# Kernel optimization log

Hardware: AMD Instinct MI355X
Metric: run time of the kernel (lower is better)

## Reference

```python
import jax, jax.numpy as jnp
import numpy as np

N_NODES = 100000
N_TYPES = 7
E_PER_TYPE = 250000
D = 128


def setup_inputs() -> dict:
    key = jax.random.key(0)
    k1, k2, k3 = jax.random.split(key, 3)
    x = jax.random.normal(k1, (N_NODES, D), dtype=jnp.float32)
    edge_index = jax.random.randint(k2, (N_TYPES, 2, E_PER_TYPE), 0, N_NODES, dtype=jnp.int64)
    # per-edge-type GNN weights (SwitchModule holds one param set per type)
    W = jax.random.normal(k3, (N_TYPES, D, D), dtype=jnp.float32) * (1.0 / np.sqrt(D))
    b = jnp.zeros((N_TYPES, D), dtype=jnp.float32)
    return {"x": x, "edge_index": edge_index, "W": W, "b": b}


def reference(x, edge_index, W, b):
    # x: [N, D]; edge_index: [T, 2, E]; W: [T, D, D]; b: [T, D]
    N = x.shape[0]
    E = edge_index.shape[-1]
    # per-type linear transform of all node features: [T, N, D]
    h = jnp.einsum('nd,tdf->tnf', x, W) + b[:, None, :]

    def per_type(ht, ei):
        src, dst = ei[0], ei[1]
        msgs = ht[src]                                   # [E, D] gather
        sums = jax.ops.segment_sum(msgs, dst, num_segments=N)
        cnt = jax.ops.segment_sum(jnp.ones((E,), ht.dtype), dst, num_segments=N)
        return sums / jnp.maximum(cnt, 1.0)[:, None]     # mean aggregation

    type_messages = jax.vmap(per_type)(h, edge_index)    # [T, N, D]
    # x_agg = sum(type_messages) / len(type_messages)
    return type_messages.mean(axis=0)
```

## Files before the change

### kernel.cpp

```cpp
#include <hip/hip_runtime.h>


constexpr int NN = 100000;
constexpr int NT = 7;
constexpr int NE = 250000;
constexpr int DD = 128;
constexpr int NROWS = ((NN + 127) / 128) * 128;
constexpr int NPART = 8;
constexpr int PSIZE = (NN + NPART - 1) / NPART;
constexpr int EPB = 1024;
constexpr int NSLAB = (NE + EPB - 1) / EPB;

typedef short bf16x8 __attribute__((ext_vector_type(8)));
typedef float f32x4 __attribute__((ext_vector_type(4)));
typedef int   i32x4 __attribute__((ext_vector_type(4)));
typedef float fltx4 __attribute__((ext_vector_type(4)));

__device__ __forceinline__ unsigned pack_bf16x2(float lo, float hi) {
    unsigned a = __float_as_uint(lo), b = __float_as_uint(hi);
    unsigned al = (a + 0x7FFFu + ((a >> 16) & 1u)) >> 16;
    unsigned bh = (b + 0x7FFFu + ((b >> 16) & 1u)) & 0xFFFF0000u;
    return al | bh;
}

__global__ __launch_bounds__(256) void convx_k(
    const float* __restrict__ x, uint4* __restrict__ xb)
{
    int id = blockIdx.x * 256 + threadIdx.x;
    const fltx4* src = (const fltx4*)x;
    fltx4 v0 = __builtin_nontemporal_load(src + (size_t)id * 2);
    fltx4 v1 = __builtin_nontemporal_load(src + (size_t)id * 2 + 1);
    uint4 o;
    o.x = pack_bf16x2(v0[0], v0[1]);
    o.y = pack_bf16x2(v0[2], v0[3]);
    o.z = pack_bf16x2(v1[0], v1[1]);
    o.w = pack_bf16x2(v1[2], v1[3]);
    xb[id] = o;
}

__global__ __launch_bounds__(256) void wconv_k(
    const float* __restrict__ W, char* __restrict__ WTb)
{
    int wid = (blockIdx.x * 256 + threadIdx.x) >> 6;
    int lane = threadIdx.x & 63;
    int t = wid >> 7, f = wid & 127;
    if (t >= NT) return;
    const float* Wt = W + (size_t)t * DD * DD;
    float w0 = Wt[(size_t)(2 * lane) * DD + f];
    float w1 = Wt[(size_t)(2 * lane + 1) * DD + f];
    int gran = (lane >> 2) ^ (f & 7);
    *(unsigned*)(WTb + (size_t)t * 32768 + f * 256 + gran * 16 + (lane & 3) * 4)
        = pack_bf16x2(w0, w1);
}

__global__ __launch_bounds__(256) void fill_k(
    const int* __restrict__ ei,
    int* __restrict__ cntT,
    int* __restrict__ eslots)
{
    int part = blockIdx.x & (NPART - 1);
    int slab = blockIdx.x >> 3;
    int t = blockIdx.y;
    int e0 = slab * EPB + threadIdx.x * 4;
    if (e0 >= NE) return;
    const int* p = ei + (size_t)t * 2 * NE;
    i32x4 s4 = __builtin_nontemporal_load((const i32x4*)(p + e0));
    i32x4 d4 = __builtin_nontemporal_load((const i32x4*)(p + NE + e0));
    int lo = part * PSIZE;
    int hi = lo + PSIZE;
    int tv = t << 17;
    #pragma unroll
    for (int k = 0; k < 4; ++k) {
        int src = s4[k];
        int dst = d4[k];
        if (dst >= lo && dst < hi) {
            int pos = atomicAdd(cntT + dst, 1);
            if (pos < 64) eslots[(size_t)dst * 64 + pos] = src | tv;
        }
    }
}

__global__ __launch_bounds__(256) void agg_k(
    const char* __restrict__ xb,
    const int* __restrict__ cntT,
    const int* __restrict__ eslots,
    char* __restrict__ aggb,
    unsigned char* __restrict__ bmask,
    int c0, int nc)
{
    int wid = (blockIdx.x * 256 + threadIdx.x) >> 6;
    int lane = threadIdx.x & 63;
    if (wid >= nc) return;
    const int n = c0 + wid;
    const bool live = (n < NN);

    int total = live ? cntT[n] : 0;
    if (total > 64) total = 64;
    int val = (live && lane < total)
            ? __builtin_nontemporal_load(eslots + (size_t)n * 64 + lane) : 0;
    int mytype = (lane < total) ? ((val >> 17) & 7) : 7;

    unsigned long long bal[8];
    #pragma unroll
    for (int t = 0; t < 8; ++t) bal[t] = __ballot(mytype == t);
    int ct[7], st[7];
    {
        int s = 0;
        #pragma unroll
        for (int t = 0; t < 7; ++t) { st[t] = s; ct[t] = (int)__popcll(bal[t]); s += ct[t]; }
    }

    unsigned long long before = 0, mine = bal[7];
    #pragma unroll
    for (int t = 0; t < 7; ++t) {
        before |= (mytype > t) ? bal[t] : 0ull;
        mine = (mytype == t) ? bal[t] : mine;
    }
    int rank = (int)__popcll(before)
             + (int)__popcll(mine & ((1ull << lane) - 1ull));
    int sorted = __builtin_amdgcn_ds_permute(rank << 2, val);
    int val2 = (lane < total) ? (sorted & 0x1FFFF) : NN;

    const int h = lane & 31;
    const int hw = lane >> 5;
    char* rowb = aggb + (size_t)(wid >> 7) * 32768 + (size_t)(wid & 127) * 256
               + (size_t)(((h >> 1) ^ (wid & 7)) << 4) + (h & 1) * 8;
    const size_t tstride = (size_t)nc * 256;
    unsigned msk = 0;

    #pragma unroll
    for (int tp = 0; tp < 7; tp += 2) {
        const int cA = ct[tp];
        const int cB = (tp + 1 < 7) ? ct[tp + 1] : 0;
        const int sA = st[tp];
        const int sB = (tp + 1 < 7) ? st[tp + 1] : 0;
        const int cM = hw ? cB : cA;
        const int sM = hw ? sB : sA;
        const int cMax = cA > cB ? cA : cB;

        float a0 = 0.f, a1 = 0.f, a2 = 0.f, a3 = 0.f;
        for (int e = 0; e < cMax; e += 2) {
            int i0 = (sM + e) & 63;
            int i1 = (sM + e + 1) & 63;
            int r0 = __shfl(val2, i0);
            int r1 = __shfl(val2, i1);
            int s0_ = (e < cM)     ? r0 : NN;
            int s1_ = (e + 1 < cM) ? r1 : NN;
            uint2 v0 = *(const uint2*)(xb + (size_t)s0_ * 256 + h * 8);
            uint2 v1 = *(const uint2*)(xb + (size_t)s1_ * 256 + h * 8);
            a0 += __uint_as_float(v0.x << 16) + __uint_as_float(v1.x << 16);
            a1 += __uint_as_float(v0.x & 0xFFFF0000u) + __uint_as_float(v1.x & 0xFFFF0000u);
            a2 += __uint_as_float(v0.y << 16) + __uint_as_float(v1.y << 16);
            a3 += __uint_as_float(v0.y & 0xFFFF0000u) + __uint_as_float(v1.y & 0xFFFF0000u);
        }
        float sc = 1.0f / fmaxf((float)cM, 1.0f);
        if (tp + hw < 7) {
            uint2 d;
            d.x = pack_bf16x2(a0 * sc, a1 * sc);
            d.y = pack_bf16x2(a2 * sc, a3 * sc);
            *(uint2*)(rowb + (size_t)(tp + hw) * tstride) = d;
        }
        msk |= (cA > 0) ? (1u << tp) : 0u;
        if (tp + 1 < 7) msk |= (cB > 0) ? (1u << (tp + 1)) : 0u;
    }
    if (live && lane == 0) bmask[n] = (unsigned char)msk;
}

__global__ __launch_bounds__(512) void gemm_k(
    const char* __restrict__ aggb, const char* __restrict__ WTb,
    const unsigned char* __restrict__ bmask, const float* __restrict__ bias,
    float* __restrict__ out, int c0, int nc)
{
    __shared__ char sA[128 * 256];
    __shared__ char sW[128 * 256];
    int tid = threadIdx.x;
    int w = tid >> 6, lane = tid & 63;
    int wy = w >> 1, wx = w & 1;
    int n0 = c0 + blockIdx.x * 128;
    const size_t tstride = (size_t)nc * 256;

    f32x4 acc[2][4];
    #pragma unroll
    for (int i = 0; i < 2; ++i)
        #pragma unroll
        for (int j = 0; j < 4; ++j) acc[i][j] = (f32x4)0.0f;

    for (int t = 0; t < NT; ++t) {
        __syncthreads();
        const char* asrc = aggb + (size_t)t * tstride + (size_t)blockIdx.x * 32768;
        const char* wsrc = WTb + (size_t)t * 32768;
        #pragma unroll
        for (int i = 0; i < 4; ++i) {
            int ch = w * 4 + i;
            __builtin_amdgcn_global_load_lds(
                (const __attribute__((address_space(1))) void*)(asrc + ch * 1024 + lane * 16),
                (__attribute__((address_space(3))) void*)(sA + ch * 1024), 16, 0, 0);
            __builtin_amdgcn_global_load_lds(
                (const __attribute__((address_space(1))) void*)(wsrc + ch * 1024 + lane * 16),
                (__attribute__((address_space(3))) void*)(sW + ch * 1024), 16, 0, 0);
        }
        __syncthreads();

        #pragma unroll
        for (int c = 0; c < 4; ++c) {
            int gsel = ((c * 4 + (lane >> 4)) ^ (lane & 7)) << 4;
            bf16x8 A0 = *(const bf16x8*)(sA + (wy * 32 + (lane & 15)) * 256 + gsel);
            bf16x8 A1 = *(const bf16x8*)(sA + (wy * 32 + 16 + (lane & 15)) * 256 + gsel);
            #pragma unroll
            for (int nj = 0; nj < 4; ++nj) {
                bf16x8 B = *(const bf16x8*)(sW + (wx * 64 + nj * 16 + (lane & 15)) * 256 + gsel);
                acc[0][nj] = __builtin_amdgcn_mfma_f32_16x16x32_bf16(A0, B, acc[0][nj], 0, 0, 0);
                acc[1][nj] = __builtin_amdgcn_mfma_f32_16x16x32_bf16(A1, B, acc[1][nj], 0, 0, 0);
            }
        }
    }

    const float inv7 = 1.0f / (float)NT;
    #pragma unroll
    for (int mi = 0; mi < 2; ++mi) {
        #pragma unroll
        for (int v = 0; v < 4; ++v) {
            int n = n0 + wy * 32 + mi * 16 + (lane >> 4) * 4 + v;
            if (n >= NN) continue;
            unsigned mk = bmask[n];
            float add[4] = {0.f, 0.f, 0.f, 0.f};
            #pragma unroll
            for (int t = 0; t < NT; ++t) {
                if ((mk >> t) & 1u) {
                    #pragma unroll
                    for (int nj = 0; nj < 4; ++nj)
                        add[nj] += bias[(size_t)t * DD + wx * 64 + nj * 16 + (lane & 15)];
                }
            }
            #pragma unroll
            for (int nj = 0; nj < 4; ++nj)
                out[(size_t)n * DD + wx * 64 + nj * 16 + (lane & 15)]
                    = inv7 * (acc[mi][nj][v] + add[nj]);
        }
    }
}

extern "C" void kernel_launch(void* const* d_in, const int* in_sizes, int n_in,
                              void* d_out, int out_size, void* d_ws, size_t ws_size,
                              hipStream_t stream) {
    const float* x  = (const float*)d_in[0];
    const int*   ei = (const int*)d_in[1];
    const float* W  = (const float*)d_in[2];
    const float* b  = (const float*)d_in[3];
    float* out = (float*)d_out;
    char* ws = (char*)d_ws;

    size_t off = 0;
    char* xb     = ws + off; off += (size_t)(NN + 1) * 256;
    char* WTb    = ws + off; off += (size_t)NT * 128 * 256;
    int*  eslots = (int*)(ws + off); off += (size_t)NN * 64 * 4;
    int*  cntT   = (int*)(ws + off); off += (size_t)NN * 4;
    unsigned char* bmask = (unsigned char*)(ws + off); off += (size_t)NN;
    off = (off + 255) & ~(size_t)255;
    char* aggb   = ws + off;

    size_t avail = (ws_size > off) ? (ws_size - off) : 0;
    int Nc = (int)(avail / ((size_t)NT * 256));
    Nc &= ~127;
    if (Nc < 128) Nc = 128;
    if (Nc > NROWS) Nc = NROWS;

    convx_k<<<(NN * DD / 8 + 255) / 256, 256, 0, stream>>>(x, (uint4*)xb);
    hipMemsetAsync(xb + (size_t)NN * 256, 0, 256, stream);
    wconv_k<<<(NT * 128 + 3) / 4, 256, 0, stream>>>(W, WTb);
    hipMemsetAsync(cntT, 0, (size_t)NN * 4, stream);
    fill_k<<<dim3(NSLAB * NPART, NT), 256, 0, stream>>>(ei, cntT, eslots);

    for (int c0 = 0; c0 < NN; c0 += Nc) {
        int nc = (NROWS - c0 < Nc) ? (NROWS - c0) : Nc;
        agg_k<<<nc / 4, 256, 0, stream>>>(xb, cntT, eslots, aggb, bmask, c0, nc);
        gemm_k<<<nc / 128, 512, 0, stream>>>(aggb, WTb, bmask, b, out, c0, nc);
    }
}
```

Baseline: 255.3 us.

## Load A tiles directly from global and double-buffer W staging in LDS

```diff
diff --git a/kernel.cpp b/kernel.cpp
--- a/kernel.cpp
+++ b/kernel.cpp
@@ -171,46 +171,55 @@
     const unsigned char* __restrict__ bmask, const float* __restrict__ bias,
     float* __restrict__ out, int c0, int nc)
 {
-    __shared__ char sA[128 * 256];
-    __shared__ char sW[128 * 256];
+    __shared__ char sW[2][128 * 256];
     int tid = threadIdx.x;
     int w = tid >> 6, lane = tid & 63;
     int wy = w >> 1, wx = w & 1;
     int n0 = c0 + blockIdx.x * 128;
     const size_t tstride = (size_t)nc * 256;
-
-    f32x4 acc[2][4];
-    #pragma unroll
-    for (int i = 0; i < 2; ++i)
-        #pragma unroll
-        for (int j = 0; j < 4; ++j) acc[i][j] = (f32x4)0.0f;
-
-    for (int t = 0; t < NT; ++t) {
-        __syncthreads();
-        const char* asrc = aggb + (size_t)t * tstride + (size_t)blockIdx.x * 32768;
+    const char* abase = aggb + (size_t)blockIdx.x * 32768;
+
+    auto stageW = [&](int buf, int t) {
         const char* wsrc = WTb + (size_t)t * 32768;
         #pragma unroll
         for (int i = 0; i < 4; ++i) {
             int ch = w * 4 + i;
             __builtin_amdgcn_global_load_lds(
-                (const __attribute__((address_space(1))) void*)(asrc + ch * 1024 + lane * 16),
-                (__attribute__((address_space(3))) void*)(sA + ch * 1024), 16, 0, 0);
-            __builtin_amdgcn_global_load_lds(
                 (const __attribute__((address_space(1))) void*)(wsrc + ch * 1024 + lane * 16),
-                (__attribute__((address_space(3))) void*)(sW + ch * 1024), 16, 0, 0);
-        }
+                (__attribute__((address_space(3))) void*)(&sW[buf][ch * 1024]), 16, 0, 0);
+        }
+    };
+
+    f32x4 acc[2][4];
+    #pragma unroll
+    for (int i = 0; i < 2; ++i)
+        #pragma unroll
+        for (int j = 0; j < 4; ++j) acc[i][j] = (f32x4)0.0f;
+
+    stageW(0, 0);
+    for (int t = 0; t < NT; ++t) {
         __syncthreads();
-
-        #pragma unroll
-        for (int c = 0; c < 4; ++c) {
-            int gsel = ((c * 4 + (lane >> 4)) ^ (lane & 7)) << 4;
-            bf16x8 A0 = *(const bf16x8*)(sA + (wy * 32 + (lane & 15)) * 256 + gsel);
-            bf16x8 A1 = *(const bf16x8*)(sA + (wy * 32 + 16 + (lane & 15)) * 256 + gsel);
+        if (t + 1 < NT) stageW((t + 1) & 1, t + 1);
+
+        const char* At = abase + (size_t)t * tstride;
+        bf16x8 A0[4], A1[4];
+        #pragma unroll
+        for (int cl = 0; cl < 4; ++cl) {
+            int gsel = ((cl * 4 + (lane >> 4)) ^ (lane & 7)) << 4;
+            const char* ar = At + (size_t)(wy * 32 + (lane & 15)) * 256 + gsel;
+            A0[cl] = *(const bf16x8*)(ar);
+            A1[cl] = *(const bf16x8*)(ar + 16 * 256);
+        }
+
+        const char* Ws = sW[t & 1];
+        #pragma unroll
+        for (int cl = 0; cl < 4; ++cl) {
+            int gsel = ((cl * 4 + (lane >> 4)) ^ (lane & 7)) << 4;
             #pragma unroll
             for (int nj = 0; nj < 4; ++nj) {
-                bf16x8 B = *(const bf16x8*)(sW + (wx * 64 + nj * 16 + (lane & 15)) * 256 + gsel);
-                acc[0][nj] = __builtin_amdgcn_mfma_f32_16x16x32_bf16(A0, B, acc[0][nj], 0, 0, 0);
-                acc[1][nj] = __builtin_amdgcn_mfma_f32_16x16x32_bf16(A1, B, acc[1][nj], 0, 0, 0);
+                bf16x8 B = *(const bf16x8*)(Ws + (wx * 64 + nj * 16 + (lane & 15)) * 256 + gsel);
+                acc[0][nj] = __builtin_amdgcn_mfma_f32_16x16x32_bf16(A0[cl], B, acc[0][nj], 0, 0, 0);
+                acc[1][nj] = __builtin_amdgcn_mfma_f32_16x16x32_bf16(A1[cl], B, acc[1][nj], 0, 0, 0);
             }
         }
     }
```

After: 258.2 us (median of 2 runs). About the same (+1.1%).
